# Kernel optimization log

Measured on AMD Instinct MI355X. Metric: run time of the kernel, lower is better.

Reference implementation:

```python
import jax, jax.numpy as jnp
import numpy as np
from math import log2, ceil

HEADS = 16
BLOCK = 16
EPS = 1e-8


def flip_every_two(t):
    # flip adjacent pairs along axis 1: (B, n, ...) with n even
    B, n = t.shape[0], t.shape[1]
    rest = t.shape[2:]
    t = t.reshape(B, n // 2, 2, *rest)
    t = jnp.flip(t, axis=2)
    return t.reshape(B, n, *rest)


def masked_aggregate(t, mask, average=True):
    # t: (B, n, 2, d), mask: (B, n, 2) bool; aggregate over axis=2
    m = mask[..., None]
    s = jnp.where(m, t, 0.0).sum(axis=2)
    total = mask.sum(axis=2)  # (B, n) int
    if average:
        s = s / jnp.clip(total, 1)[..., None].astype(t.dtype)
    return jnp.where((total == 0)[..., None], 0.0, s)


def _forward(x, Wq, bq, Wk, bk, Wv, bv, mask):
    b, n, hidden = x.shape
    h, bsz, d = HEADS, BLOCK, hidden // HEADS
    scale = d ** -0.5
    pad_to_len = 2 ** ceil(log2(n))
    pad = pad_to_len - n
    if pad != 0:
        x = jnp.pad(x, ((0, 0), (0, pad), (0, 0)))
        mask = jnp.pad(mask, ((0, 0), (0, pad)), constant_values=False)
    N = pad_to_len

    def split_heads(t):  # (b, N, h*d) -> (b*h, N, d)
        return t.reshape(b, N, h, d).transpose(0, 2, 1, 3).reshape(b * h, N, d)

    q = split_heads(x @ Wq + bq) * scale
    k = split_heads(x @ Wk + bk)
    v = split_heads(x @ Wv + bv)
    m = jnp.broadcast_to(mask[:, None, :], (b, h, N)).reshape(b * h, N)

    num_levels = int(log2(N // bsz)) - 2
    qkvs = [(q, k, v, m)]
    for _ in range(num_levels):
        B, L, _ = q.shape
        q2 = q.reshape(B, L // 2, 2, d)
        k2 = k.reshape(B, L // 2, 2, d)
        v2 = v.reshape(B, L // 2, 2, d)
        m2 = m.reshape(B, L // 2, 2)
        q = masked_aggregate(q2, m2, average=True)
        k = masked_aggregate(k2, m2, average=True)
        v = masked_aggregate(v2, m2, average=False)
        m = jnp.any(m2, axis=2)
        qkvs.append((q, k, v, m))
    qkvs = [qkvs[0]] + qkvs

    Ys = []
    for ind, (ql, kl, vl, ml) in enumerate(reversed(qkvs)):
        is_last = ind == len(qkvs) - 1
        B, L, _ = ql.shape
        nb = L // bsz
        qb = ql.reshape(B, nb, bsz, d)
        kb = kl.reshape(B, nb, bsz, d)
        vb = vl.reshape(B, nb, bsz, d)
        mb = ml.reshape(B, nb, bsz)
        k_mask = mb if is_last else flip_every_two(mb)
        S_mask = mb[..., :, None] & k_mask[..., None, :]  # (B, nb, bsz, bsz)
        if not is_last:
            kb = flip_every_two(kb)
            vb = flip_every_two(vb)
        S = jnp.einsum('bnid,bnjd->bnij', qb, kb)
        S = jnp.where(S_mask, S, jnp.finfo(S.dtype).min)
        S = S - S.max(axis=-1, keepdims=True)
        A = jnp.exp(S)
        Y = jnp.einsum('bnij,bnjd->bnid', A, vb)
        Ys.append((Y.reshape(B, L, d), A.sum(axis=-1).reshape(B, L)))

    Y, A = Ys[0]
    for ind in range(1, len(Ys)):
        is_last = ind == len(Ys) - 1
        if not is_last:
            Y = jnp.repeat(Y, 2, axis=1)
            A = jnp.repeat(A, 2, axis=1)
        Y = Ys[ind][0] + Y
        A = Ys[ind][1] + A

    out = Y / (A + EPS)[..., None]  # (b*h, N, d)
    out = out.reshape(b, h, N, d).transpose(0, 2, 1, 3).reshape(b, N, hidden)
    return out[:, :n]


def setup_inputs():
    key = jax.random.key(0)
    ks = jax.random.split(key, 7)
    b, n, hidden = 2, 8192, 1024
    s = 1.0 / np.sqrt(hidden)
    x = jax.random.normal(ks[0], (b, n, hidden), jnp.float32)
    mask = jnp.ones((b, n), dtype=bool)
    Wq = jax.random.normal(ks[1], (hidden, hidden), jnp.float32) * s
    Wk = jax.random.normal(ks[2], (hidden, hidden), jnp.float32) * s
    Wv = jax.random.normal(ks[3], (hidden, hidden), jnp.float32) * s
    bq = jax.random.normal(ks[4], (hidden,), jnp.float32) * 0.01
    bk = jax.random.normal(ks[5], (hidden,), jnp.float32) * 0.01
    bv = jax.random.normal(ks[6], (hidden,), jnp.float32) * 0.01
    return {"x": x, "mask": mask, "Wq": Wq, "bq": bq, "Wk": Wk, "bk": bk, "Wv": Wv, "bv": bv}


def reference(x, mask, Wq, bq, Wk, bk, Wv, bv):
    return _forward(x, Wq, bq, Wk, bk, Wv, bv, mask)
```

## Files before the change

kernel.cpp:

```cpp
#include <hip/hip_runtime.h>
#include <hip/hip_bf16.h>

typedef __attribute__((ext_vector_type(4))) float f32x4;
typedef __attribute__((ext_vector_type(8))) __bf16 bf16x8;
typedef __attribute__((ext_vector_type(4))) unsigned int u32x4;

#define TE 33423360ull

__device__ __forceinline__ unsigned short f2b_rne(float f) {
  unsigned u = __float_as_uint(f);
  return (unsigned short)((u + 0x7fffu + ((u >> 16) & 1u)) >> 16);
}
__device__ __forceinline__ float b2f(unsigned s) { return __uint_as_float(s << 16); }

__device__ __forceinline__ void gload_lds16(const unsigned short* g, unsigned short* l) {
  __builtin_amdgcn_global_load_lds((const __attribute__((address_space(1))) void*)g,
                                   (__attribute__((address_space(3))) void*)l, 16, 0, 0);
}

__global__ void conv_x(const float* __restrict__ x, unsigned short* __restrict__ xb) {
  size_t i = ((size_t)blockIdx.x * 256 + threadIdx.x) * 8;
  f32x4 A = *(const f32x4*)(x + i);
  f32x4 B = *(const f32x4*)(x + i + 4);
  u32x4 o;
  o[0] = f2b_rne(A[0]) | ((unsigned)f2b_rne(A[1]) << 16);
  o[1] = f2b_rne(A[2]) | ((unsigned)f2b_rne(A[3]) << 16);
  o[2] = f2b_rne(B[0]) | ((unsigned)f2b_rne(B[1]) << 16);
  o[3] = f2b_rne(B[2]) | ((unsigned)f2b_rne(B[3]) << 16);
  *(u32x4*)(xb + i) = o;
}

__global__ void transpose_w(const float* __restrict__ Wq, const float* __restrict__ Wk,
                            const float* __restrict__ Wv, unsigned short* __restrict__ wt) {
  int z = blockIdx.z;
  const float* W = (z == 0) ? Wq : (z == 1) ? Wk : Wv;
  __shared__ float t[32][33];
  int n0 = blockIdx.x * 32, k0 = blockIdx.y * 32;
  int tx = threadIdx.x, ty = threadIdx.y;
#pragma unroll
  for (int j = 0; j < 4; ++j)
    t[ty + j * 8][tx] = W[(size_t)(k0 + ty + j * 8) * 1024 + n0 + tx];
  __syncthreads();
  unsigned short* o = wt + (size_t)z * 1048576;
#pragma unroll
  for (int j = 0; j < 4; ++j)
    o[(size_t)(n0 + ty + j * 8) * 1024 + k0 + tx] = f2b_rne(t[tx][ty + j * 8]);
}

__global__ __launch_bounds__(256, 2) void gemm_qkv(
    const unsigned short* __restrict__ xb, const unsigned short* __restrict__ wt,
    const float* __restrict__ bq, const float* __restrict__ bk, const float* __restrict__ bv,
    unsigned short* __restrict__ qkv) {
  int flat = blockIdx.y * 8 + blockIdx.x;
  int swz = (flat & 7) * 128 + (flat >> 3);
  int m0 = (swz >> 3) * 128, n0 = (swz & 7) * 128;
  __shared__ unsigned short lds[32768];
  int tid = threadIdx.x;
  int lane = tid & 63, wid = tid >> 6;
  int g = lane >> 4, r16 = lane & 15;
  int wm = (wid >> 1) * 64, wn = (wid & 1) * 64;
  int srow = wid * 16 + (lane >> 2);
  int sc8 = ((lane & 3) ^ ((lane >> 3) & 3)) * 8;

  auto stage = [&](int b, int kt) {
    unsigned short* Tb = lds + b * 16384;
    int kc = kt * 32 + sc8;
#pragma unroll
    for (int a = 0; a < 2; ++a) {
      gload_lds16(xb + (size_t)(m0 + a * 64 + srow) * 1024 + kc, Tb + a * 2048 + wid * 512);
#pragma unroll
      for (int z = 0; z < 3; ++z)
        gload_lds16(wt + (size_t)z * 1048576 + (size_t)(n0 + a * 64 + srow) * 1024 + kc,
                    Tb + 4096 + z * 4096 + a * 2048 + wid * 512);
    }
  };

  f32x4 acc[3][4][4];
#pragma unroll
  for (int z = 0; z < 3; ++z)
#pragma unroll
    for (int i = 0; i < 4; ++i)
#pragma unroll
      for (int j = 0; j < 4; ++j) acc[z][i][j] = (f32x4){0.f, 0.f, 0.f, 0.f};

  int slot8 = (g ^ ((r16 >> 1) & 3)) * 8;

  stage(0, 0);
  stage(1, 1);
  for (int kt = 0; kt < 32; ++kt) {
    int cb = kt & 1;
    if (kt < 31) asm volatile("s_waitcnt vmcnt(8)" ::: "memory");
    else         asm volatile("s_waitcnt vmcnt(0)" ::: "memory");
    __builtin_amdgcn_s_barrier();
    __builtin_amdgcn_sched_barrier(0);
    const unsigned short* Tb = lds + cb * 16384;
    bf16x8 af[4];
#pragma unroll
    for (int t = 0; t < 4; ++t)
      af[t] = *(const bf16x8*)(Tb + (wm + t * 16 + r16) * 32 + slot8);
#pragma unroll
    for (int z = 0; z < 3; ++z) {
      bf16x8 bf_[4];
#pragma unroll
      for (int t = 0; t < 4; ++t)
        bf_[t] = *(const bf16x8*)(Tb + 4096 + z * 4096 + (wn + t * 16 + r16) * 32 + slot8);
#pragma unroll
      for (int i = 0; i < 4; ++i)
#pragma unroll
        for (int j = 0; j < 4; ++j)
          acc[z][i][j] = __builtin_amdgcn_mfma_f32_16x16x32_bf16(af[i], bf_[j], acc[z][i][j], 0, 0, 0);
    }
    __builtin_amdgcn_sched_barrier(0);
    __builtin_amdgcn_s_barrier();
    if (kt < 30) stage(cb, kt + 2);
  }

  unsigned short* Ct = lds;
#pragma unroll
  for (int z = 0; z < 3; ++z) {
    const float* bias = (z == 0) ? bq : (z == 1) ? bk : bv;
    float scale = (z == 0) ? 0.125f : 1.0f;
#pragma unroll
    for (int pass = 0; pass < 2; ++pass) {
      __syncthreads();
      if ((wid >> 1) == pass) {
#pragma unroll
        for (int i = 0; i < 4; ++i) {
#pragma unroll
          for (int j = 0; j < 4; ++j) {
            int col = wn + j * 16 + r16;
            float bc = bias[n0 + col];
#pragma unroll
            for (int r = 0; r < 4; ++r) {
              int rl = i * 16 + g * 4 + r;
              Ct[rl * 144 + col] = f2b_rne((acc[z][i][j][r] + bc) * scale);
            }
          }
        }
      }
      __syncthreads();
      int rl = tid >> 2, q = tid & 3;
      int R = m0 + pass * 64 + rl;
      int colg = n0 + q * 32;
      int bh = ((R >> 13) << 4) + (colg >> 6);
      unsigned short* op =
          qkv + (size_t)z * TE + ((size_t)bh * 8192 + (size_t)(R & 8191)) * 64 + (q & 1) * 32;
#pragma unroll
      for (int ch = 0; ch < 4; ++ch)
        *(u32x4*)(op + ch * 8) = *(const u32x4*)(Ct + rl * 144 + q * 32 + ch * 8);
    }
  }
}

__global__ __launch_bounds__(256) void agg_all(unsigned short* __restrict__ qkv) {
  int seg = blockIdx.x, bh = blockIdx.y, z = blockIdx.z;
  unsigned short* tb = qkv + (size_t)z * TE;
  __shared__ unsigned short b0[16384];
  __shared__ unsigned short b1[8192];
  int t = threadIdx.x;
  const unsigned short* ip = tb + ((size_t)bh * 8192 + (size_t)seg * 256) * 64;
#pragma unroll
  for (int j = 0; j < 8; ++j)
    *(u32x4*)(b0 + (j * 256 + t) * 8) = *(const u32x4*)(ip + (size_t)(j * 256 + t) * 8);
  __syncthreads();
  float sc = (z < 2) ? 0.5f : 1.0f;
  long off = 8192;
  unsigned short* src = b0;
  unsigned short* dst = b1;
  for (int l = 1; l <= 7; ++l) {
    int R = 256 >> l;
    int chunks = R * 32;
    for (int c = t; c < chunks; c += 256) {
      int r = c >> 5, cc = c & 31;
      unsigned a = *(const unsigned*)(src + (2 * r) * 64 + cc * 2);
      unsigned b = *(const unsigned*)(src + (2 * r + 1) * 64 + cc * 2);
      float lo = (b2f(a & 0xffffu) + b2f(b & 0xffffu)) * sc;
      float hi = (b2f(a >> 16) + b2f(b >> 16)) * sc;
      unsigned o = f2b_rne(lo) | ((unsigned)f2b_rne(hi) << 16);
      *(unsigned*)(dst + r * 64 + cc * 2) = o;
      unsigned short* op =
          tb + (size_t)off * 2048 + ((size_t)bh * (8192 >> l) + (size_t)seg * R + r) * 64;
      *(unsigned*)(op + cc * 2) = o;
    }
    __syncthreads();
    off += 8192 >> l;
    unsigned short* tmp = src; src = dst; dst = tmp;
  }
}

union U8 { bf16x8 v; unsigned short u[8]; };

__device__ __forceinline__ void attn_unit(
    const unsigned short* kb, const unsigned short* vb, bf16x8 qf0, bf16x8 qf1,
    int g, int qr, f32x4 (&acc)[4], float& aacc) {
  bf16x8 kf0 = *(const bf16x8*)(kb + qr * 64 + g * 8);
  bf16x8 kf1 = *(const bf16x8*)(kb + qr * 64 + 32 + g * 8);
  f32x4 s = {0.f, 0.f, 0.f, 0.f};
  s = __builtin_amdgcn_mfma_f32_16x16x32_bf16(kf0, qf0, s, 0, 0, 0);
  s = __builtin_amdgcn_mfma_f32_16x16x32_bf16(kf1, qf1, s, 0, 0, 0);
  float mx = fmaxf(fmaxf(s[0], s[1]), fmaxf(s[2], s[3]));
  mx = fmaxf(mx, __shfl_xor(mx, 16));
  mx = fmaxf(mx, __shfl_xor(mx, 32));
  float av[4], asum = 0.f;
#pragma unroll
  for (int r = 0; r < 4; ++r) { av[r] = __expf(s[r] - mx); asum += av[r]; }
  asum += __shfl_xor(asum, 16);
  asum += __shfl_xor(asum, 32);
  aacc += asum;
  U8 A_;
#pragma unroll
  for (int r = 0; r < 4; ++r) A_.u[r] = f2b_rne(av[r]);
#pragma unroll
  for (int r = 4; r < 8; ++r) A_.u[r] = 0;
#pragma unroll
  for (int cg = 0; cg < 4; ++cg) {
    int c = cg * 16 + qr;
    U8 B_;
#pragma unroll
    for (int r = 0; r < 4; ++r) B_.u[r] = vb[(g * 4 + r) * 64 + c];
#pragma unroll
    for (int r = 4; r < 8; ++r) B_.u[r] = 0;
    acc[cg] = __builtin_amdgcn_mfma_f32_16x16x32_bf16(A_.v, B_.v, acc[cg], 0, 0, 0);
  }
}

__global__ __launch_bounds__(64) void attn_fused(const unsigned short* __restrict__ qkv,
                                                 float* __restrict__ outp) {
  int flat = blockIdx.y * 512 + blockIdx.x;
  int fb = (flat & 7) * 2048 + (flat >> 3);
  int bh = fb >> 9, B0 = fb & 511;
  int lane = threadIdx.x;
  int g = lane >> 4, qr = lane & 15;
  const unsigned short* qt = qkv;
  const unsigned short* kt = qkv + TE;
  const unsigned short* vt = qkv + 2 * TE;
  f32x4 acc[4];
#pragma unroll
  for (int cg = 0; cg < 4; ++cg) acc[cg] = (f32x4){0.f, 0.f, 0.f, 0.f};
  float aacc = 0.f;
  int off = 0;
#pragma unroll
  for (int l = 0; l <= 7; ++l) {
    int L = 8192 >> l;
    size_t base = (size_t)off * 2048 + (size_t)bh * L * 64;
    const unsigned short* qb = qt + base;
    const unsigned short* kb = kt + base;
    const unsigned short* vb = vt + base;
    int qrow = (B0 * 16 + qr) >> l;
    bf16x8 qf0 = *(const bf16x8*)(qb + (size_t)qrow * 64 + g * 8);
    bf16x8 qf1 = *(const bf16x8*)(qb + (size_t)qrow * 64 + 32 + g * 8);
    int P = B0 >> l;
    if (l == 0) {
      attn_unit(kb + (size_t)P * 1024, vb + (size_t)P * 1024, qf0, qf1, g, qr, acc, aacc);
      attn_unit(kb + (size_t)(P ^ 1) * 1024, vb + (size_t)(P ^ 1) * 1024, qf0, qf1, g, qr, acc, aacc);
    } else {
      int S_ = P ^ 1;
      attn_unit(kb + (size_t)S_ * 1024, vb + (size_t)S_ * 1024, qf0, qf1, g, qr, acc, aacc);
    }
    off += L;
  }
  int b_ = bh >> 4, h_ = bh & 15;
#pragma unroll
  for (int r = 0; r < 4; ++r) {
    int p = g * 4 + r;
    float ap = __shfl(aacc, p);
    float inv = 1.0f / (ap + 1e-8f);
    float* od = outp + ((size_t)(b_ * 8192 + B0 * 16 + p)) * 1024 + h_ * 64 + qr;
#pragma unroll
    for (int cg = 0; cg < 4; ++cg) od[cg * 16] = acc[cg][r] * inv;
  }
}

extern "C" void kernel_launch(void* const* d_in, const int* in_sizes, int n_in,
                              void* d_out, int out_size, void* d_ws, size_t ws_size,
                              hipStream_t stream) {
  const float* x = (const float*)d_in[0];
  const float* Wq = (const float*)d_in[2];
  const float* bq = (const float*)d_in[3];
  const float* Wk = (const float*)d_in[4];
  const float* bk = (const float*)d_in[5];
  const float* Wv = (const float*)d_in[6];
  const float* bv = (const float*)d_in[7];
  float* out = (float*)d_out;

  char* ws = (char*)d_ws;
  size_t o = 0;
  unsigned short* qkv = (unsigned short*)(ws + o); o += 200540160ull;
  unsigned short* wt = (unsigned short*)(ws + o); o += 6291456ull;
  unsigned short* xb = (unsigned short*)(ws + o); o += 33554432ull;
  if (ws_size < o) return;

  conv_x<<<8192, 256, 0, stream>>>(x, xb);
  transpose_w<<<dim3(32, 32, 3), dim3(32, 8), 0, stream>>>(Wq, Wk, Wv, wt);
  gemm_qkv<<<dim3(8, 128), 256, 0, stream>>>(xb, wt, bq, bk, bv, qkv);
  agg_all<<<dim3(32, 32, 3), 256, 0, stream>>>(qkv);
  attn_fused<<<dim3(512, 32), 64, 0, stream>>>(qkv, out);
}
```

Measured before the change: 250.0 us.

## Store V transposed (d-major) to vectorize V fragment loads in attention

The projection epilogue now writes V in a transposed per-head layout (dim-major, position contiguous). The aggregation kernel gains a separate path that sums adjacent positions along the contiguous axis for this layout. In the attention kernel, each lane then loads four consecutive V values with one 8-byte load instead of four strided 2-byte loads. The cost is scattered 2-byte LDS reads in the V epilogue and narrower global stores in the V aggregation.

New measurement: 293.1 us. 1.17x slower.

```diff
diff --git a/kernel.cpp b/kernel.cpp
--- a/kernel.cpp
+++ b/kernel.cpp
@@ -4,6 +4,7 @@
 typedef __attribute__((ext_vector_type(4))) float f32x4;
 typedef __attribute__((ext_vector_type(8))) __bf16 bf16x8;
 typedef __attribute__((ext_vector_type(4))) unsigned int u32x4;
+typedef __attribute__((ext_vector_type(4))) unsigned short u16x4;
 
 #define TE 33423360ull
 
@@ -139,15 +140,36 @@
         }
       }
       __syncthreads();
-      int rl = tid >> 2, q = tid & 3;
-      int R = m0 + pass * 64 + rl;
-      int colg = n0 + q * 32;
-      int bh = ((R >> 13) << 4) + (colg >> 6);
-      unsigned short* op =
-          qkv + (size_t)z * TE + ((size_t)bh * 8192 + (size_t)(R & 8191)) * 64 + (q & 1) * 32;
-#pragma unroll
-      for (int ch = 0; ch < 4; ++ch)
-        *(u32x4*)(op + ch * 8) = *(const u32x4*)(Ct + rl * 144 + q * 32 + ch * 8);
+      if (z < 2) {
+        int rl = tid >> 2, q = tid & 3;
+        int R = m0 + pass * 64 + rl;
+        int colg = n0 + q * 32;
+        int bh = ((R >> 13) << 4) + (colg >> 6);
+        unsigned short* op =
+            qkv + (size_t)z * TE + ((size_t)bh * 8192 + (size_t)(R & 8191)) * 64 + (q & 1) * 32;
+#pragma unroll
+        for (int ch = 0; ch < 4; ++ch)
+          *(u32x4*)(op + ch * 8) = *(const u32x4*)(Ct + rl * 144 + q * 32 + ch * 8);
+      } else {
+        int col = tid >> 1, pb = (tid & 1) * 32;
+        int h = (n0 + col) >> 6, dd = (n0 + col) & 63;
+        int bh = ((m0 >> 13) << 4) + h;
+        int pos0 = (m0 & 8191) + pass * 64 + pb;
+        unsigned short* vp =
+            qkv + 2 * TE + (size_t)bh * 524288 + (size_t)dd * 8192 + pos0;
+#pragma unroll
+        for (int cch = 0; cch < 4; ++cch) {
+          u32x4 ov;
+#pragma unroll
+          for (int w = 0; w < 4; ++w) {
+            int p0 = pb + cch * 8 + w * 2;
+            unsigned lo = Ct[p0 * 144 + col];
+            unsigned hi = Ct[(p0 + 1) * 144 + col];
+            ov[w] = lo | (hi << 16);
+          }
+          *(u32x4*)(vp + cch * 8) = ov;
+        }
+      }
     }
   }
 }
@@ -158,41 +180,73 @@
   __shared__ unsigned short b0[16384];
   __shared__ unsigned short b1[8192];
   int t = threadIdx.x;
-  const unsigned short* ip = tb + ((size_t)bh * 8192 + (size_t)seg * 256) * 64;
-#pragma unroll
-  for (int j = 0; j < 8; ++j)
-    *(u32x4*)(b0 + (j * 256 + t) * 8) = *(const u32x4*)(ip + (size_t)(j * 256 + t) * 8);
-  __syncthreads();
-  float sc = (z < 2) ? 0.5f : 1.0f;
-  long off = 8192;
-  unsigned short* src = b0;
-  unsigned short* dst = b1;
-  for (int l = 1; l <= 7; ++l) {
-    int R = 256 >> l;
-    int chunks = R * 32;
-    for (int c = t; c < chunks; c += 256) {
-      int r = c >> 5, cc = c & 31;
-      unsigned a = *(const unsigned*)(src + (2 * r) * 64 + cc * 2);
-      unsigned b = *(const unsigned*)(src + (2 * r + 1) * 64 + cc * 2);
-      float lo = (b2f(a & 0xffffu) + b2f(b & 0xffffu)) * sc;
-      float hi = (b2f(a >> 16) + b2f(b >> 16)) * sc;
-      unsigned o = f2b_rne(lo) | ((unsigned)f2b_rne(hi) << 16);
-      *(unsigned*)(dst + r * 64 + cc * 2) = o;
-      unsigned short* op =
-          tb + (size_t)off * 2048 + ((size_t)bh * (8192 >> l) + (size_t)seg * R + r) * 64;
-      *(unsigned*)(op + cc * 2) = o;
-    }
+  if (z < 2) {
+    const unsigned short* ip = tb + ((size_t)bh * 8192 + (size_t)seg * 256) * 64;
+#pragma unroll
+    for (int j = 0; j < 8; ++j)
+      *(u32x4*)(b0 + (j * 256 + t) * 8) = *(const u32x4*)(ip + (size_t)(j * 256 + t) * 8);
     __syncthreads();
-    off += 8192 >> l;
-    unsigned short* tmp = src; src = dst; dst = tmp;
+    float sc = 0.5f;
+    long off = 8192;
+    unsigned short* src = b0;
+    unsigned short* dst = b1;
+    for (int l = 1; l <= 7; ++l) {
+      int R = 256 >> l;
+      int chunks = R * 32;
+      for (int c = t; c < chunks; c += 256) {
+        int r = c >> 5, cc = c & 31;
+        unsigned a = *(const unsigned*)(src + (2 * r) * 64 + cc * 2);
+        unsigned b = *(const unsigned*)(src + (2 * r + 1) * 64 + cc * 2);
+        float lo = (b2f(a & 0xffffu) + b2f(b & 0xffffu)) * sc;
+        float hi = (b2f(a >> 16) + b2f(b >> 16)) * sc;
+        unsigned o = f2b_rne(lo) | ((unsigned)f2b_rne(hi) << 16);
+        *(unsigned*)(dst + r * 64 + cc * 2) = o;
+        unsigned short* op =
+            tb + (size_t)off * 2048 + ((size_t)bh * (8192 >> l) + (size_t)seg * R + r) * 64;
+        *(unsigned*)(op + cc * 2) = o;
+      }
+      __syncthreads();
+      off += 8192 >> l;
+      unsigned short* tmp = src; src = dst; dst = tmp;
+    }
+  } else {
+    const unsigned short* ipT = tb + (size_t)bh * 524288 + (size_t)seg * 256;
+#pragma unroll
+    for (int j = 0; j < 8; ++j) {
+      int e = j * 2048 + t * 8;
+      int d = e >> 8, pos = e & 255;
+      *(u32x4*)(b0 + d * 256 + pos) = *(const u32x4*)(ipT + (size_t)d * 8192 + pos);
+    }
+    __syncthreads();
+    long off = 8192;
+    unsigned short* src = b0;
+    unsigned short* dst = b1;
+    int Lc = 256;
+    for (int l = 1; l <= 7; ++l) {
+      int R = Lc >> 1;
+      int items = 64 * R;
+      int Ll = 8192 >> l;
+      int rsh = 8 - l;
+      for (int c = t; c < items; c += 256) {
+        int d = c >> rsh, p = c & (R - 1);
+        unsigned a = *(const unsigned*)(src + d * Lc + 2 * p);
+        unsigned short o = f2b_rne(b2f(a & 0xffffu) + b2f(a >> 16));
+        dst[d * R + p] = o;
+        tb[(size_t)off * 2048 + (size_t)bh * 64 * Ll + (size_t)d * Ll + (size_t)seg * R + p] = o;
+      }
+      __syncthreads();
+      off += Ll;
+      Lc = R;
+      unsigned short* tmp = src; src = dst; dst = tmp;
+    }
   }
 }
 
 union U8 { bf16x8 v; unsigned short u[8]; };
 
 __device__ __forceinline__ void attn_unit(
-    const unsigned short* kb, const unsigned short* vb, bf16x8 qf0, bf16x8 qf1,
-    int g, int qr, f32x4 (&acc)[4], float& aacc) {
+    const unsigned short* kb, const unsigned short* vcol, int L,
+    bf16x8 qf0, bf16x8 qf1, int g, int qr, f32x4 (&acc)[4], float& aacc) {
   bf16x8 kf0 = *(const bf16x8*)(kb + qr * 64 + g * 8);
   bf16x8 kf1 = *(const bf16x8*)(kb + qr * 64 + 32 + g * 8);
   f32x4 s = {0.f, 0.f, 0.f, 0.f};
@@ -214,10 +268,10 @@
   for (int r = 4; r < 8; ++r) A_.u[r] = 0;
 #pragma unroll
   for (int cg = 0; cg < 4; ++cg) {
-    int c = cg * 16 + qr;
+    u16x4 vv = *(const u16x4*)(vcol + (size_t)(cg * 16 + qr) * L + g * 4);
     U8 B_;
 #pragma unroll
-    for (int r = 0; r < 4; ++r) B_.u[r] = vb[(g * 4 + r) * 64 + c];
+    for (int r = 0; r < 4; ++r) B_.u[r] = vv[r];
 #pragma unroll
     for (int r = 4; r < 8; ++r) B_.u[r] = 0;
     acc[cg] = __builtin_amdgcn_mfma_f32_16x16x32_bf16(A_.v, B_.v, acc[cg], 0, 0, 0);
@@ -251,11 +305,11 @@
     bf16x8 qf1 = *(const bf16x8*)(qb + (size_t)qrow * 64 + 32 + g * 8);
     int P = B0 >> l;
     if (l == 0) {
-      attn_unit(kb + (size_t)P * 1024, vb + (size_t)P * 1024, qf0, qf1, g, qr, acc, aacc);
-      attn_unit(kb + (size_t)(P ^ 1) * 1024, vb + (size_t)(P ^ 1) * 1024, qf0, qf1, g, qr, acc, aacc);
+      attn_unit(kb + (size_t)P * 1024, vb + P * 16, L, qf0, qf1, g, qr, acc, aacc);
+      attn_unit(kb + (size_t)(P ^ 1) * 1024, vb + (P ^ 1) * 16, L, qf0, qf1, g, qr, acc, aacc);
     } else {
       int S_ = P ^ 1;
-      attn_unit(kb + (size_t)S_ * 1024, vb + (size_t)S_ * 1024, qf0, qf1, g, qr, acc, aacc);
+      attn_unit(kb + (size_t)S_ * 1024, vb + S_ * 16, L, qf0, qf1, g, qr, acc, aacc);
     }
     off += L;
   }
```
